# Kernel tuning notes

Hardware: AMD Instinct MI355X
Metric: run time of the kernel (lower is better)

## Reference

```python
import jax, jax.numpy as jnp
import numpy as np

D, HS, HE, E, K = 1024, 2048, 1024, 8, 2   # d_model, shared hidden (d_ff//2), expert hidden (d_ff//4), n_experts, top_k
B, T = 4, 1024
N_SHARED = 1


def setup_inputs() -> dict:
    key = jax.random.key(0)
    ks = jax.random.split(key, 9)
    g = lambda k, shape, s: jax.random.normal(k, shape, jnp.float32) * s
    return {
        "x": g(ks[0], (B, T, D), 1.0),
        "t_emb": g(ks[1], (B, D), 1.0),
        "router_W": g(ks[2], (2 * D, E), 0.01),      # torch Linear(2C->E, bias=False), std=0.01 init
        "router_bias": jnp.zeros((E,), jnp.float32),  # load-balance bias buffer
        "w1": g(ks[3], (D, HS), 0.02),                # shared expert SwiGLU
        "w3": g(ks[4], (D, HS), 0.02),
        "w2": g(ks[5], (HS, D), 0.02),
        "W1e": g(ks[6], (E, D, HE), 0.02),            # routed experts, Linear->GELU->Linear
        "W2e": g(ks[7], (E, HE, D), 0.02),
    }


def reference(x, t_emb, router_W, router_bias, w1, w3, w2, W1e, W2e):
    Bb, Tt, C = x.shape
    xf = x.reshape(-1, C)                                              # [N, C]
    tf = jnp.broadcast_to(t_emb[:, None, :], (Bb, Tt, C)).reshape(-1, C)
    N = xf.shape[0]

    shared = (jax.nn.silu(xf @ w1) * (xf @ w3)) @ w2                   # [N, C]

    # router affinity (sigmoid, fp32)
    s = jax.nn.sigmoid((jnp.concatenate([xf, tf], axis=-1) @ router_W).astype(jnp.float32))
    sel_scores = s + router_bias                                       # [N, E]
    _, topk_idx = jax.lax.top_k(sel_scores, K)                         # [N, K]

    # gates normalized over selected raw affinities
    s_sel = jnp.take_along_axis(s, topk_idx, axis=1)                   # [N, K]
    denom = s_sel.sum(axis=1, keepdims=True)
    gates = jnp.where(denom > 1e-9, s_sel / (denom + 1e-9), 1.0 / K).astype(x.dtype)

    # combine weights [N, E]: scatter gates to selected experts
    combine = jnp.zeros((N, E), x.dtype).at[jnp.arange(N)[:, None], topk_idx].add(gates)

    # dense expert evaluation (reference form of grouped GEMM + scatter-combine)
    h = jax.nn.gelu(jnp.einsum('nc,ech->enh', xf, W1e), approximate=False)  # [E, N, He]
    y = jnp.einsum('enh,ehc->enc', h, W2e)                                   # [E, N, C]
    routed = jnp.einsum('ne,enc->nc', combine, y)                            # [N, C]

    return ((shared + routed) / (N_SHARED + K)).reshape(Bb, Tt, C)
```

## Files before the change

kernel.cpp:

```cpp
#include <hip/hip_runtime.h>
#include <hip/hip_bf16.h>
#include <math.h>

#define D_MODEL 1024
#define HS 2048
#define HE 1024
#define NEXP 8
#define NTOK 4096
#define NSLOT 8192

typedef __attribute__((ext_vector_type(4))) float f32x4;
typedef __attribute__((ext_vector_type(8))) short bf16x8;

__device__ __forceinline__ short f2b(float f) {
  __hip_bfloat16 h = __float2bfloat16(f);
  return *reinterpret_cast<short*>(&h);
}
__device__ __forceinline__ float b2f(short s) {
  return __bfloat162float(*reinterpret_cast<__hip_bfloat16*>(&s));
}

__device__ __forceinline__ void gl_lds16(const short* g, short* l) {
  __builtin_amdgcn_global_load_lds(
      (const __attribute__((address_space(1))) void*)g,
      (__attribute__((address_space(3))) void*)l, 16, 0, 0);
}

__device__ __forceinline__ void tr_tile(const float* __restrict__ in,
                                        short* __restrict__ out, int R, int C,
                                        int bx, int by, int bz, int rmap,
                                        float (*tile)[69], int t) {
  const int c0 = bx * 64;
  const int r0 = by * 64;
  const size_t bo = (size_t)bz * R * C;
  const int lr = t >> 4;
  const int lc4 = (t & 15) * 4;
#pragma unroll
  for (int i = 0; i < 4; i++) {
    const float4 v = *(const float4*)&in[bo + (size_t)(r0 + lr + i * 16) * C + c0 + lc4];
    tile[lc4 + 0][lr + i * 16] = v.x;
    tile[lc4 + 1][lr + i * 16] = v.y;
    tile[lc4 + 2][lr + i * 16] = v.z;
    tile[lc4 + 3][lr + i * 16] = v.w;
  }
  __syncthreads();
#pragma unroll
  for (int i = 0; i < 4; i++) {
    const int oc = (t >> 4) + i * 16;
    const int or4 = (t & 15) * 4;
    short4 o;
    o.x = f2b(tile[oc][or4 + 0]);
    o.y = f2b(tile[oc][or4 + 1]);
    o.z = f2b(tile[oc][or4 + 2]);
    o.w = f2b(tile[oc][or4 + 3]);
    const int c = c0 + oc;
    size_t orow;
    if (rmap == 0) orow = bo + (size_t)c * R;
    else orow = (size_t)((c >> 5) * 64 + (rmap == 2 ? 32 : 0) + (c & 31)) * R;
    *(short4*)&out[orow + r0 + or4] = o;
  }
}

__global__ __launch_bounds__(256) void tr_w13(const float* __restrict__ w1,
                                              const float* __restrict__ w3,
                                              short* __restrict__ w13I) {
  __shared__ float tile[64][69];
  const int z = blockIdx.z;
  tr_tile(z ? w3 : w1, w13I, D_MODEL, HS, blockIdx.x, blockIdx.y, 0, z ? 2 : 1,
          tile, threadIdx.x);
}

__global__ __launch_bounds__(256) void tr_w2(const float* __restrict__ w2,
                                             short* __restrict__ w2T) {
  __shared__ float tile[64][69];
  tr_tile(w2, w2T, HS, D_MODEL, blockIdx.x, blockIdx.y, 0, 0, tile, threadIdx.x);
}

__global__ __launch_bounds__(256) void tr_exp(const float* __restrict__ W1e,
                                              const float* __restrict__ W2e,
                                              short* __restrict__ W1eT,
                                              short* __restrict__ W2eT) {
  __shared__ float tile[64][69];
  const int z = blockIdx.z;
  if (z < 8)
    tr_tile(W1e, W1eT, D_MODEL, HE, blockIdx.x, blockIdx.y, z, 0, tile, threadIdx.x);
  else
    tr_tile(W2e, W2eT, HE, D_MODEL, blockIdx.x, blockIdx.y, z - 8, 0, tile, threadIdx.x);
}

__global__ __launch_bounds__(256) void router_kernel(
    const float* __restrict__ x, const float* __restrict__ temb,
    const float* __restrict__ rw, const float* __restrict__ rbias,
    short* __restrict__ xb, int* __restrict__ topk, float* __restrict__ gates) {
  const int t = (blockIdx.x * 256 + threadIdx.x) >> 6;
  const int lane = threadIdx.x & 63;
  const float* xr = x + (size_t)t * D_MODEL;
  const float* tr = temb + (size_t)(t >> 10) * D_MODEL;
  float acc[NEXP] = {};
#pragma unroll
  for (int i = 0; i < 4; i++) {
    const int j = i * 256 + lane * 4;
    const float4 xv = *(const float4*)&xr[j];
    const float4 tv = *(const float4*)&tr[j];
    short4 o;
    o.x = f2b(xv.x); o.y = f2b(xv.y); o.z = f2b(xv.z); o.w = f2b(xv.w);
    *(short4*)&xb[(size_t)t * D_MODEL + j] = o;
    const float* wx = rw + (size_t)j * NEXP;
    const float* wt = rw + (size_t)(D_MODEL + j) * NEXP;
    const float xa[4] = {xv.x, xv.y, xv.z, xv.w};
    const float ta[4] = {tv.x, tv.y, tv.z, tv.w};
#pragma unroll
    for (int u = 0; u < 4; u++)
#pragma unroll
      for (int e = 0; e < NEXP; e++)
        acc[e] += xa[u] * wx[u * NEXP + e] + ta[u] * wt[u * NEXP + e];
  }
#pragma unroll
  for (int off = 32; off; off >>= 1)
#pragma unroll
    for (int e = 0; e < NEXP; e++) acc[e] += __shfl_xor(acc[e], off);
  if (lane == 0) {
    float s[NEXP], sel[NEXP];
#pragma unroll
    for (int e = 0; e < NEXP; e++) {
      s[e] = 1.f / (1.f + expf(-acc[e]));
      sel[e] = s[e] + rbias[e];
    }
    int i0 = 0;
#pragma unroll
    for (int e = 1; e < NEXP; e++) if (sel[e] > sel[i0]) i0 = e;
    int i1 = (i0 == 0) ? 1 : 0;
#pragma unroll
    for (int e = 0; e < NEXP; e++) if (e != i0 && sel[e] > sel[i1]) i1 = e;
    float s0 = s[i0], s1 = s[i1], den = s0 + s1;
    float g0, g1;
    if (den > 1e-9f) { g0 = s0 / (den + 1e-9f); g1 = s1 / (den + 1e-9f); }
    else { g0 = 0.5f; g1 = 0.5f; }
    topk[t * 2] = i0; topk[t * 2 + 1] = i1;
    gates[t * 2] = g0; gates[t * 2 + 1] = g1;
  }
}

__global__ __launch_bounds__(1024) void group_kernel(const int* __restrict__ topk,
                                                     int* __restrict__ perm,
                                                     int* __restrict__ offs,
                                                     int* __restrict__ te,
                                                     int* __restrict__ tm,
                                                     int* __restrict__ ntile) {
  __shared__ int cnt[NEXP], cur[NEXP];
  const int t = threadIdx.x;
  if (t < NEXP) cnt[t] = 0;
  __syncthreads();
  int mye[8];
#pragma unroll
  for (int i = 0; i < 8; i++) {
    mye[i] = topk[i * 1024 + t];
    atomicAdd(&cnt[mye[i]], 1);
  }
  __syncthreads();
  if (t == 0) {
    int a = 0;
    for (int e = 0; e < NEXP; e++) { offs[e] = a; cur[e] = a; a += cnt[e]; }
    offs[NEXP] = a;
    int nt = 0;
    for (int e = 0; e < NEXP; e++)
      for (int m0 = 0; m0 < cnt[e]; m0 += 256) { te[nt] = e; tm[nt] = m0; nt++; }
    ntile[0] = nt;
  }
  __syncthreads();
#pragma unroll
  for (int i = 0; i < 8; i++) {
    int pos = atomicAdd(&cur[mye[i]], 1);
    perm[pos] = i * 1024 + t;
  }
}

template <int MODE>
__global__ __launch_bounds__(512, 1) void moe_gemm_8ph(
    const short* __restrict__ A, const short* __restrict__ B, short* __restrict__ Cout,
    const int* __restrict__ perm, const int* __restrict__ offs,
    const float* __restrict__ gates, const int* __restrict__ te,
    const int* __restrict__ tm, const int* __restrict__ ntile) {
  extern __shared__ short lds[];
  const int td = threadIdx.x;
  int bx, m0, rbeg = 0, rend = 0;
  const short* Bbase;
  if (MODE == 0) {
    const int id = blockIdx.x, xcd = id & 7, slot = id >> 3;
    bx = (xcd & 3) * 4 + (slot & 3);
    m0 = ((xcd >> 2) * 8 + (slot >> 2)) * 256;
    Bbase = B + (size_t)bx * 256 * 1024;
  } else {
    const int id = blockIdx.x;
    const int work = (id & 7) * 20 + (id >> 3);
    const int ty = work >> 2;
    if (ty >= ntile[0]) return;
    bx = work & 3;
    const int e = te[ty];
    m0 = tm[ty];
    rbeg = offs[e]; rend = offs[e + 1];
    Bbase = B + ((size_t)e * 1024 + bx * 256) * 1024;
  }

  const int srow = td >> 3;
  const int colsw8 = ((td & 7) ^ (srow & 7)) * 8;
  const short* ap[2][2];
  const short* bp[2][2];
#pragma unroll
  for (int h = 0; h < 2; h++)
#pragma unroll
    for (int i = 0; i < 2; i++) {
      const int trow = h * 128 + i * 64 + srow;
      int grow;
      if (MODE == 0) grow = m0 + trow;
      else if (MODE == 1) grow = perm[min(rbeg + m0 + trow, rend - 1)] >> 1;
      else grow = min(rbeg + m0 + trow, rend - 1);
      ap[h][i] = A + (size_t)grow * 1024 + colsw8;
      bp[h][i] = Bbase + (size_t)trow * 1024 + colsw8;
    }

#define SU1(t_, b_)                                                        \
  do {                                                                     \
    gl_lds16(bp[0][0] + (t_) * 64, lds + (b_) * 32768 + 16384 + td * 8);   \
    gl_lds16(bp[0][1] + (t_) * 64, lds + (b_) * 32768 + 16384 + 4096 + td * 8); \
  } while (0)
#define SU2(t_, b_)                                                        \
  do {                                                                     \
    gl_lds16(bp[1][0] + (t_) * 64, lds + (b_) * 32768 + 16384 + 8192 + td * 8); \
    gl_lds16(bp[1][1] + (t_) * 64, lds + (b_) * 32768 + 16384 + 8192 + 4096 + td * 8); \
  } while (0)
#define SU3(t_, b_)                                                        \
  do {                                                                     \
    gl_lds16(ap[0][0] + (t_) * 64, lds + (b_) * 32768 + td * 8);           \
    gl_lds16(ap[1][0] + (t_) * 64, lds + (b_) * 32768 + 8192 + td * 8);    \
  } while (0)
#define SU4(t_, b_)                                                        \
  do {                                                                     \
    gl_lds16(ap[0][1] + (t_) * 64, lds + (b_) * 32768 + 4096 + td * 8);    \
    gl_lds16(ap[1][1] + (t_) * 64, lds + (b_) * 32768 + 8192 + 4096 + td * 8); \
  } while (0)

  const int l = td & 63;
  const int wid = td >> 6;
  const int mh = wid >> 2;
  const int wn4 = wid & 3;
  const int lr = l & 15;
  const int bhsel = wn4 >> 1;
  const int bnr = (wn4 & 1) * 64;
  const int swzk0 = ((0 + (l >> 4) * 16) ^ ((l & 7) << 4)) >> 1;
  const int swzk1 = ((64 + (l >> 4) * 16) ^ ((l & 7) << 4)) >> 1;

#define LDA(mf_, swz_) (*(const bf16x8*)&Ah[(unsigned)(((mf_)*16 + lr) * 64) + (swz_)])
#define LDB(nf_, swz_) (*(const bf16x8*)&Bh[(unsigned)((bnr + (nf_)*16 + lr) * 64) + (swz_)])
#define MMROW(mf_, a_)                                                                 \
  acc[mf_][0] = __builtin_amdgcn_mfma_f32_16x16x32_bf16(a_, b0, acc[mf_][0], 0, 0, 0); \
  acc[mf_][1] = __builtin_amdgcn_mfma_f32_16x16x32_bf16(a_, b1, acc[mf_][1], 0, 0, 0); \
  acc[mf_][2] = __builtin_amdgcn_mfma_f32_16x16x32_bf16(a_, b2, acc[mf_][2], 0, 0, 0); \
  acc[mf_][3] = __builtin_amdgcn_mfma_f32_16x16x32_bf16(a_, b3, acc[mf_][3], 0, 0, 0)

#define PH_TAIL                                   \
  __builtin_amdgcn_s_barrier();                   \
  __builtin_amdgcn_s_setprio(1)
#define PH_END                                    \
  __builtin_amdgcn_s_setprio(0);                  \
  __builtin_amdgcn_s_barrier()

  f32x4 acc[8][4] = {};

  SU1(0, 0); SU2(0, 0); SU3(0, 0); SU4(0, 0);
  asm volatile("s_waitcnt vmcnt(2)" ::: "memory");
  __builtin_amdgcn_s_barrier();

  for (int t = 0; t < 16; ++t) {
    const int p = t & 1, q = p ^ 1;
    const short* Ah = lds + p * 32768 + mh * 8192;
    const short* Bh = lds + p * 32768 + 16384 + bhsel * 8192;
    bf16x8 b0, b1, b2, b3, a0, a1, a2, a3;
    b0 = LDB(0, swzk0); b1 = LDB(1, swzk0); b2 = LDB(2, swzk0); b3 = LDB(3, swzk0);
    a0 = LDA(0, swzk0); a1 = LDA(1, swzk0); a2 = LDA(2, swzk0); a3 = LDA(3, swzk0);
    if (t < 15) {
      SU1(t + 1, q); SU2(t + 1, q);
      asm volatile("s_waitcnt vmcnt(4)" ::: "memory");
    } else {
      asm volatile("s_waitcnt vmcnt(0)" ::: "memory");
    }
    PH_TAIL;
    MMROW(0, a0); MMROW(1, a1); MMROW(2, a2); MMROW(3, a3);
    PH_END;
    a0 = LDA(4, swzk0); a1 = LDA(5, swzk0); a2 = LDA(6, swzk0); a3 = LDA(7, swzk0);
    if (t < 15) { SU3(t + 1, q); SU4(t + 1, q); }
    PH_TAIL;
    MMROW(4, a0); MMROW(5, a1); MMROW(6, a2); MMROW(7, a3);
    PH_END;
    b0 = LDB(0, swzk1); b1 = LDB(1, swzk1); b2 = LDB(2, swzk1); b3 = LDB(3, swzk1);
    a0 = LDA(0, swzk1); a1 = LDA(1, swzk1); a2 = LDA(2, swzk1); a3 = LDA(3, swzk1);
    PH_TAIL;
    MMROW(0, a0); MMROW(1, a1); MMROW(2, a2); MMROW(3, a3);
    PH_END;
    a0 = LDA(4, swzk1); a1 = LDA(5, swzk1); a2 = LDA(6, swzk1); a3 = LDA(7, swzk1);
    if (t < 15) asm volatile("s_waitcnt vmcnt(2)" ::: "memory");
    PH_TAIL;
    MMROW(4, a0); MMROW(5, a1); MMROW(6, a2); MMROW(7, a3);
    PH_END;
  }

  const int rsub = (l >> 4) * 4;
  if (MODE == 0) {
#pragma unroll
    for (int mf = 0; mf < 8; mf++)
#pragma unroll
      for (int j = 0; j < 4; j++) {
        const int row = m0 + mh * 128 + mf * 16 + rsub + j;
        short* Up = Cout + (size_t)row * HS + bx * 128 + wn4 * 32 + lr;
#pragma unroll
        for (int nfp = 0; nfp < 2; nfp++) {
          const float a = acc[mf][nfp][j];
          const float b = acc[mf][nfp + 2][j];
          Up[nfp * 16] = f2b(a / (1.f + expf(-a)) * b);
        }
      }
  } else if (MODE == 1) {
#pragma unroll
    for (int mf = 0; mf < 8; mf++)
#pragma unroll
      for (int j = 0; j < 4; j++) {
        const int gi = rbeg + m0 + mh * 128 + mf * 16 + rsub + j;
        if (gi < rend) {
          short* Cp = Cout + (size_t)gi * HE + bx * 256 + wn4 * 64 + lr;
#pragma unroll
          for (int nf = 0; nf < 4; nf++) {
            const float v = acc[mf][nf][j];
            Cp[nf * 16] = f2b(0.5f * v * (1.0f + erff(v * 0.70710678118654752f)));
          }
        }
      }
  } else {
#pragma unroll
    for (int mf = 0; mf < 8; mf++)
#pragma unroll
      for (int j = 0; j < 4; j++) {
        const int gi = rbeg + m0 + mh * 128 + mf * 16 + rsub + j;
        if (gi < rend) {
          const int slot = perm[gi];
          const float g = gates[slot];
          short* Cp = Cout + (size_t)slot * D_MODEL + bx * 256 + wn4 * 64 + lr;
#pragma unroll
          for (int nf = 0; nf < 4; nf++) Cp[nf * 16] = f2b(g * acc[mf][nf][j]);
        }
      }
  }
#undef SU1
#undef SU2
#undef SU3
#undef SU4
#undef LDA
#undef LDB
#undef MMROW
#undef PH_TAIL
#undef PH_END
}

__global__ __launch_bounds__(256, 2) void gemm_g2(
    const short* __restrict__ A, const short* __restrict__ B,
    const short* __restrict__ yb, float* __restrict__ out) {
  __shared__ __align__(16) short As[4096];
  __shared__ __align__(16) short Bs[4096];
  const int t = threadIdx.x;
  const int id = blockIdx.x, xcd = id & 7, slot = id >> 3;
  const int tile_n = (slot & 7) * 128;
  const int m0 = (xcd * 4 + (slot >> 3)) * 128;
  const int r = t >> 2;
  const int c8 = (t & 3) * 8;
  const short* Ap0 = A + (size_t)(m0 + r) * HS + c8;
  const short* Ap1 = A + (size_t)(m0 + 64 + r) * HS + c8;
  const short* Bp0 = B + (size_t)(tile_n + r) * HS + c8;
  const short* Bp1 = B + (size_t)(tile_n + 64 + r) * HS + c8;

  const int lane = t & 63, wv = t >> 6;
  const int wm = (wv >> 1) * 64, wn = (wv & 1) * 64;
  const int lr = lane & 15, lk = (lane >> 4) * 8;

  f32x4 acc[4][4] = {};
  for (int k0 = 0; k0 < HS; k0 += 32) {
    gl_lds16(Ap0 + k0, &As[t * 8]);
    gl_lds16(Ap1 + k0, &As[2048 + t * 8]);
    gl_lds16(Bp0 + k0, &Bs[t * 8]);
    gl_lds16(Bp1 + k0, &Bs[2048 + t * 8]);
    __syncthreads();
    bf16x8 af[4], bfr[4];
#pragma unroll
    for (int m = 0; m < 4; m++) af[m] = *(const bf16x8*)&As[(wm + m * 16 + lr) * 32 + lk];
#pragma unroll
    for (int n = 0; n < 4; n++) bfr[n] = *(const bf16x8*)&Bs[(wn + n * 16 + lr) * 32 + lk];
#pragma unroll
    for (int m = 0; m < 4; m++)
#pragma unroll
      for (int n = 0; n < 4; n++)
        acc[m][n] = __builtin_amdgcn_mfma_f32_16x16x32_bf16(af[m], bfr[n], acc[m][n], 0, 0, 0);
    __syncthreads();
  }

  const int rq = (lane >> 4) * 4;
  const float inv3 = 1.0f / 3.0f;
#pragma unroll
  for (int m = 0; m < 4; m++) {
#pragma unroll
    for (int j = 0; j < 4; j++) {
      const int tok = m0 + wm + m * 16 + rq + j;
      const int colb = tile_n + wn + lr;
      const short* y0p = yb + (size_t)(tok * 2) * D_MODEL + colb;
      const short* y1p = yb + (size_t)(tok * 2 + 1) * D_MODEL + colb;
      float* Op = out + (size_t)tok * D_MODEL + colb;
#pragma unroll
      for (int n = 0; n < 4; n++) {
        Op[n * 16] = (acc[m][n][j] + b2f(y0p[n * 16]) + b2f(y1p[n * 16])) * inv3;
      }
    }
  }
}

extern "C" void kernel_launch(void* const* d_in, const int* in_sizes, int n_in,
                              void* d_out, int out_size, void* d_ws, size_t ws_size,
                              hipStream_t stream) {
  const float* x = (const float*)d_in[0];
  const float* temb = (const float*)d_in[1];
  const float* rw = (const float*)d_in[2];
  const float* rbias = (const float*)d_in[3];
  const float* w1 = (const float*)d_in[4];
  const float* w3 = (const float*)d_in[5];
  const float* w2 = (const float*)d_in[6];
  const float* W1e = (const float*)d_in[7];
  const float* W2e = (const float*)d_in[8];
  float* out = (float*)d_out;

  const size_t MB = 1ull << 20;
  char* w = (char*)d_ws;
  short* xb    = (short*)(w + 0 * MB);
  short* w13I  = (short*)(w + 8 * MB);
  short* w2T   = (short*)(w + 16 * MB);
  short* W1eT  = (short*)(w + 20 * MB);
  short* W2eT  = (short*)(w + 36 * MB);
  short* ubuf  = (short*)(w + 52 * MB);
  short* hexpb = (short*)(w + 68 * MB);
  short* yb    = (short*)(w + 84 * MB);
  float* gates = (float*)(w + 100 * MB);
  int* topk    = (int*)(w + 100 * MB + 32 * 1024);
  int* perm    = (int*)(w + 100 * MB + 64 * 1024);
  int* meta    = (int*)(w + 100 * MB + 96 * 1024);
  int* offs    = meta;
  int* te      = meta + 16;
  int* tm      = meta + 128;
  int* ntile   = meta + 256;

  hipFuncSetAttribute((const void*)&moe_gemm_8ph<0>,
                      hipFuncAttributeMaxDynamicSharedMemorySize, 131072);
  hipFuncSetAttribute((const void*)&moe_gemm_8ph<1>,
                      hipFuncAttributeMaxDynamicSharedMemorySize, 131072);
  hipFuncSetAttribute((const void*)&moe_gemm_8ph<2>,
                      hipFuncAttributeMaxDynamicSharedMemorySize, 131072);

  tr_w13<<<dim3(HS / 64, D_MODEL / 64, 2), 256, 0, stream>>>(w1, w3, w13I);
  tr_w2<<<dim3(D_MODEL / 64, HS / 64, 1), 256, 0, stream>>>(w2, w2T);
  tr_exp<<<dim3(16, 16, 16), 256, 0, stream>>>(W1e, W2e, W1eT, W2eT);
  router_kernel<<<NTOK / 4, 256, 0, stream>>>(x, temb, rw, rbias, xb, topk, gates);
  group_kernel<<<1, 1024, 0, stream>>>(topk, perm, offs, te, tm, ntile);

  moe_gemm_8ph<0><<<256, 512, 131072, stream>>>(xb, w13I, ubuf, nullptr, nullptr,
                                                nullptr, nullptr, nullptr, nullptr);

  moe_gemm_8ph<1><<<160, 512, 131072, stream>>>(xb, W1eT, hexpb, perm, offs,
                                                gates, te, tm, ntile);
  moe_gemm_8ph<2><<<160, 512, 131072, stream>>>(hexpb, W2eT, yb, perm, offs,
                                                gates, te, tm, ntile);

  gemm_g2<<<256, 256, 0, stream>>>(ubuf, w2T, yb, out);
}
```

Baseline: 236.3 us.

## Restructure GEMM pipelines: coarse per-tile staging and double-buffered swizzled final GEMM

The main MoE GEMM kernel drops its 8-phase interleaved schedule, with barriers after every MFMA group. It now issues all global-to-LDS loads for the next K tile up front, uses one barrier per tile, and runs the MFMA phases without intermediate barriers. The final shared-expert down-projection GEMM is rewritten from a single-buffered 32-wide K loop with two __syncthreads per step into a double-buffered 64-wide K loop with XOR-swizzled LDS and the same coarse staging. This removes barrier overhead and adds load/compute overlap in the final GEMM. In exchange, the finer load/MFMA interleaving in the main kernel is lost, and the final GEMM needs 64KB of dynamic LDS.

```diff
diff --git a/kernel.cpp b/kernel.cpp
--- a/kernel.cpp
+++ b/kernel.cpp
@@ -176,7 +176,7 @@
 }
 
 template <int MODE>
-__global__ __launch_bounds__(512, 1) void moe_gemm_8ph(
+__global__ __launch_bounds__(512, 1) void moe_gemm_ct(
     const short* __restrict__ A, const short* __restrict__ B, short* __restrict__ Cout,
     const int* __restrict__ perm, const int* __restrict__ offs,
     const float* __restrict__ gates, const int* __restrict__ te,
@@ -219,25 +219,16 @@
       bp[h][i] = Bbase + (size_t)trow * 1024 + colsw8;
     }
 
-#define SU1(t_, b_)                                                        \
-  do {                                                                     \
-    gl_lds16(bp[0][0] + (t_) * 64, lds + (b_) * 32768 + 16384 + td * 8);   \
+#define STAGE_ALL(t_, b_)                                                       \
+  do {                                                                          \
+    gl_lds16(bp[0][0] + (t_) * 64, lds + (b_) * 32768 + 16384 + td * 8);        \
     gl_lds16(bp[0][1] + (t_) * 64, lds + (b_) * 32768 + 16384 + 4096 + td * 8); \
-  } while (0)
-#define SU2(t_, b_)                                                        \
-  do {                                                                     \
     gl_lds16(bp[1][0] + (t_) * 64, lds + (b_) * 32768 + 16384 + 8192 + td * 8); \
-    gl_lds16(bp[1][1] + (t_) * 64, lds + (b_) * 32768 + 16384 + 8192 + 4096 + td * 8); \
-  } while (0)
-#define SU3(t_, b_)                                                        \
-  do {                                                                     \
-    gl_lds16(ap[0][0] + (t_) * 64, lds + (b_) * 32768 + td * 8);           \
-    gl_lds16(ap[1][0] + (t_) * 64, lds + (b_) * 32768 + 8192 + td * 8);    \
-  } while (0)
-#define SU4(t_, b_)                                                        \
-  do {                                                                     \
-    gl_lds16(ap[0][1] + (t_) * 64, lds + (b_) * 32768 + 4096 + td * 8);    \
-    gl_lds16(ap[1][1] + (t_) * 64, lds + (b_) * 32768 + 8192 + 4096 + td * 8); \
+    gl_lds16(bp[1][1] + (t_) * 64, lds + (b_) * 32768 + 16384 + 12288 + td * 8);\
+    gl_lds16(ap[0][0] + (t_) * 64, lds + (b_) * 32768 + td * 8);                \
+    gl_lds16(ap[0][1] + (t_) * 64, lds + (b_) * 32768 + 4096 + td * 8);         \
+    gl_lds16(ap[1][0] + (t_) * 64, lds + (b_) * 32768 + 8192 + td * 8);         \
+    gl_lds16(ap[1][1] + (t_) * 64, lds + (b_) * 32768 + 12288 + td * 8);        \
   } while (0)
 
   const int l = td & 63;
@@ -258,50 +249,44 @@
   acc[mf_][2] = __builtin_amdgcn_mfma_f32_16x16x32_bf16(a_, b2, acc[mf_][2], 0, 0, 0); \
   acc[mf_][3] = __builtin_amdgcn_mfma_f32_16x16x32_bf16(a_, b3, acc[mf_][3], 0, 0, 0)
 
-#define PH_TAIL                                   \
-  __builtin_amdgcn_s_barrier();                   \
-  __builtin_amdgcn_s_setprio(1)
-#define PH_END                                    \
-  __builtin_amdgcn_s_setprio(0);                  \
-  __builtin_amdgcn_s_barrier()
-
   f32x4 acc[8][4] = {};
 
-  SU1(0, 0); SU2(0, 0); SU3(0, 0); SU4(0, 0);
-  asm volatile("s_waitcnt vmcnt(2)" ::: "memory");
-  __builtin_amdgcn_s_barrier();
+  STAGE_ALL(0, 0);
 
   for (int t = 0; t < 16; ++t) {
     const int p = t & 1, q = p ^ 1;
     const short* Ah = lds + p * 32768 + mh * 8192;
     const short* Bh = lds + p * 32768 + 16384 + bhsel * 8192;
-    bf16x8 b0, b1, b2, b3, a0, a1, a2, a3;
-    b0 = LDB(0, swzk0); b1 = LDB(1, swzk0); b2 = LDB(2, swzk0); b3 = LDB(3, swzk0);
-    a0 = LDA(0, swzk0); a1 = LDA(1, swzk0); a2 = LDA(2, swzk0); a3 = LDA(3, swzk0);
     if (t < 15) {
-      SU1(t + 1, q); SU2(t + 1, q);
-      asm volatile("s_waitcnt vmcnt(4)" ::: "memory");
+      STAGE_ALL(t + 1, q);
+      asm volatile("s_waitcnt vmcnt(8)" ::: "memory");
     } else {
       asm volatile("s_waitcnt vmcnt(0)" ::: "memory");
     }
-    PH_TAIL;
-    MMROW(0, a0); MMROW(1, a1); MMROW(2, a2); MMROW(3, a3);
-    PH_END;
-    a0 = LDA(4, swzk0); a1 = LDA(5, swzk0); a2 = LDA(6, swzk0); a3 = LDA(7, swzk0);
-    if (t < 15) { SU3(t + 1, q); SU4(t + 1, q); }
-    PH_TAIL;
-    MMROW(4, a0); MMROW(5, a1); MMROW(6, a2); MMROW(7, a3);
-    PH_END;
-    b0 = LDB(0, swzk1); b1 = LDB(1, swzk1); b2 = LDB(2, swzk1); b3 = LDB(3, swzk1);
-    a0 = LDA(0, swzk1); a1 = LDA(1, swzk1); a2 = LDA(2, swzk1); a3 = LDA(3, swzk1);
-    PH_TAIL;
-    MMROW(0, a0); MMROW(1, a1); MMROW(2, a2); MMROW(3, a3);
-    PH_END;
-    a0 = LDA(4, swzk1); a1 = LDA(5, swzk1); a2 = LDA(6, swzk1); a3 = LDA(7, swzk1);
-    if (t < 15) asm volatile("s_waitcnt vmcnt(2)" ::: "memory");
-    PH_TAIL;
-    MMROW(4, a0); MMROW(5, a1); MMROW(6, a2); MMROW(7, a3);
-    PH_END;
+    __builtin_amdgcn_s_barrier();
+    {
+      bf16x8 b0, b1, b2, b3, a0, a1, a2, a3;
+      b0 = LDB(0, swzk0); b1 = LDB(1, swzk0); b2 = LDB(2, swzk0); b3 = LDB(3, swzk0);
+      a0 = LDA(0, swzk0); a1 = LDA(1, swzk0); a2 = LDA(2, swzk0); a3 = LDA(3, swzk0);
+      __builtin_amdgcn_s_setprio(1);
+      MMROW(0, a0); MMROW(1, a1); MMROW(2, a2); MMROW(3, a3);
+      __builtin_amdgcn_s_setprio(0);
+      a0 = LDA(4, swzk0); a1 = LDA(5, swzk0); a2 = LDA(6, swzk0); a3 = LDA(7, swzk0);
+      __builtin_amdgcn_s_setprio(1);
+      MMROW(4, a0); MMROW(5, a1); MMROW(6, a2); MMROW(7, a3);
+      __builtin_amdgcn_s_setprio(0);
+      b0 = LDB(0, swzk1); b1 = LDB(1, swzk1); b2 = LDB(2, swzk1); b3 = LDB(3, swzk1);
+      a0 = LDA(0, swzk1); a1 = LDA(1, swzk1); a2 = LDA(2, swzk1); a3 = LDA(3, swzk1);
+      __builtin_amdgcn_s_setprio(1);
+      MMROW(0, a0); MMROW(1, a1); MMROW(2, a2); MMROW(3, a3);
+      __builtin_amdgcn_s_setprio(0);
+      a0 = LDA(4, swzk1); a1 = LDA(5, swzk1); a2 = LDA(6, swzk1); a3 = LDA(7, swzk1);
+      __builtin_amdgcn_s_setprio(1);
+      MMROW(4, a0); MMROW(5, a1); MMROW(6, a2); MMROW(7, a3);
+      __builtin_amdgcn_s_setprio(0);
+    }
+    __builtin_amdgcn_sched_barrier(0);
+    __builtin_amdgcn_s_barrier();
   }
 
   const int rsub = (l >> 4) * 4;
@@ -349,58 +334,90 @@
         }
       }
   }
-#undef SU1
-#undef SU2
-#undef SU3
-#undef SU4
+#undef STAGE_ALL
 #undef LDA
 #undef LDB
 #undef MMROW
-#undef PH_TAIL
-#undef PH_END
-}
-
-__global__ __launch_bounds__(256, 2) void gemm_g2(
+}
+
+__global__ __launch_bounds__(256, 2) void gemm_g2_ct(
     const short* __restrict__ A, const short* __restrict__ B,
     const short* __restrict__ yb, float* __restrict__ out) {
-  __shared__ __align__(16) short As[4096];
-  __shared__ __align__(16) short Bs[4096];
-  const int t = threadIdx.x;
+  extern __shared__ short lds[];
+  const int td = threadIdx.x;
   const int id = blockIdx.x, xcd = id & 7, slot = id >> 3;
   const int tile_n = (slot & 7) * 128;
   const int m0 = (xcd * 4 + (slot >> 3)) * 128;
-  const int r = t >> 2;
-  const int c8 = (t & 3) * 8;
-  const short* Ap0 = A + (size_t)(m0 + r) * HS + c8;
-  const short* Ap1 = A + (size_t)(m0 + 64 + r) * HS + c8;
-  const short* Bp0 = B + (size_t)(tile_n + r) * HS + c8;
-  const short* Bp1 = B + (size_t)(tile_n + 64 + r) * HS + c8;
-
-  const int lane = t & 63, wv = t >> 6;
+
+  const int srow = td >> 3;
+  const int colsw8 = ((td & 7) ^ (srow & 7)) * 8;
+  const short* ap[4];
+  const short* bp[4];
+#pragma unroll
+  for (int u = 0; u < 4; u++) {
+    ap[u] = A + (size_t)(m0 + u * 32 + srow) * HS + colsw8;
+    bp[u] = B + (size_t)(tile_n + u * 32 + srow) * HS + colsw8;
+  }
+
+#define STAGE_ALL2(t_, b_)                                                 \
+  do {                                                                     \
+    gl_lds16(ap[0] + (t_) * 64, lds + (b_) * 16384 + td * 8);              \
+    gl_lds16(ap[1] + (t_) * 64, lds + (b_) * 16384 + 2048 + td * 8);       \
+    gl_lds16(ap[2] + (t_) * 64, lds + (b_) * 16384 + 4096 + td * 8);       \
+    gl_lds16(ap[3] + (t_) * 64, lds + (b_) * 16384 + 6144 + td * 8);       \
+    gl_lds16(bp[0] + (t_) * 64, lds + (b_) * 16384 + 8192 + td * 8);       \
+    gl_lds16(bp[1] + (t_) * 64, lds + (b_) * 16384 + 10240 + td * 8);      \
+    gl_lds16(bp[2] + (t_) * 64, lds + (b_) * 16384 + 12288 + td * 8);      \
+    gl_lds16(bp[3] + (t_) * 64, lds + (b_) * 16384 + 14336 + td * 8);      \
+  } while (0)
+
+  const int l = td & 63;
+  const int wv = td >> 6;
   const int wm = (wv >> 1) * 64, wn = (wv & 1) * 64;
-  const int lr = lane & 15, lk = (lane >> 4) * 8;
+  const int lr = l & 15;
+  const int swzk0 = ((0 + (l >> 4) * 16) ^ ((l & 7) << 4)) >> 1;
+  const int swzk1 = ((64 + (l >> 4) * 16) ^ ((l & 7) << 4)) >> 1;
+
+#define LDA2(mf_, swz_) (*(const bf16x8*)&Ah[(unsigned)(((mf_)*16 + lr) * 64) + (swz_)])
+#define LDB2(nf_, swz_) (*(const bf16x8*)&Bh[(unsigned)(((nf_)*16 + lr) * 64) + (swz_)])
+#define MMROW2(mf_, a_)                                                                \
+  acc[mf_][0] = __builtin_amdgcn_mfma_f32_16x16x32_bf16(a_, b0, acc[mf_][0], 0, 0, 0); \
+  acc[mf_][1] = __builtin_amdgcn_mfma_f32_16x16x32_bf16(a_, b1, acc[mf_][1], 0, 0, 0); \
+  acc[mf_][2] = __builtin_amdgcn_mfma_f32_16x16x32_bf16(a_, b2, acc[mf_][2], 0, 0, 0); \
+  acc[mf_][3] = __builtin_amdgcn_mfma_f32_16x16x32_bf16(a_, b3, acc[mf_][3], 0, 0, 0)
 
   f32x4 acc[4][4] = {};
-  for (int k0 = 0; k0 < HS; k0 += 32) {
-    gl_lds16(Ap0 + k0, &As[t * 8]);
-    gl_lds16(Ap1 + k0, &As[2048 + t * 8]);
-    gl_lds16(Bp0 + k0, &Bs[t * 8]);
-    gl_lds16(Bp1 + k0, &Bs[2048 + t * 8]);
-    __syncthreads();
-    bf16x8 af[4], bfr[4];
-#pragma unroll
-    for (int m = 0; m < 4; m++) af[m] = *(const bf16x8*)&As[(wm + m * 16 + lr) * 32 + lk];
-#pragma unroll
-    for (int n = 0; n < 4; n++) bfr[n] = *(const bf16x8*)&Bs[(wn + n * 16 + lr) * 32 + lk];
-#pragma unroll
-    for (int m = 0; m < 4; m++)
-#pragma unroll
-      for (int n = 0; n < 4; n++)
-        acc[m][n] = __builtin_amdgcn_mfma_f32_16x16x32_bf16(af[m], bfr[n], acc[m][n], 0, 0, 0);
-    __syncthreads();
-  }
-
-  const int rq = (lane >> 4) * 4;
+
+  STAGE_ALL2(0, 0);
+  for (int t = 0; t < 32; ++t) {
+    const int p = t & 1, q = p ^ 1;
+    const short* Ah = lds + p * 16384 + wm * 64;
+    const short* Bh = lds + p * 16384 + 8192 + wn * 64;
+    if (t < 31) {
+      STAGE_ALL2(t + 1, q);
+      asm volatile("s_waitcnt vmcnt(8)" ::: "memory");
+    } else {
+      asm volatile("s_waitcnt vmcnt(0)" ::: "memory");
+    }
+    __builtin_amdgcn_s_barrier();
+    {
+      bf16x8 b0, b1, b2, b3, a0, a1, a2, a3;
+      b0 = LDB2(0, swzk0); b1 = LDB2(1, swzk0); b2 = LDB2(2, swzk0); b3 = LDB2(3, swzk0);
+      a0 = LDA2(0, swzk0); a1 = LDA2(1, swzk0); a2 = LDA2(2, swzk0); a3 = LDA2(3, swzk0);
+      __builtin_amdgcn_s_setprio(1);
+      MMROW2(0, a0); MMROW2(1, a1); MMROW2(2, a2); MMROW2(3, a3);
+      __builtin_amdgcn_s_setprio(0);
+      b0 = LDB2(0, swzk1); b1 = LDB2(1, swzk1); b2 = LDB2(2, swzk1); b3 = LDB2(3, swzk1);
+      a0 = LDA2(0, swzk1); a1 = LDA2(1, swzk1); a2 = LDA2(2, swzk1); a3 = LDA2(3, swzk1);
+      __builtin_amdgcn_s_setprio(1);
+      MMROW2(0, a0); MMROW2(1, a1); MMROW2(2, a2); MMROW2(3, a3);
+      __builtin_amdgcn_s_setprio(0);
+    }
+    __builtin_amdgcn_sched_barrier(0);
+    __builtin_amdgcn_s_barrier();
+  }
+
+  const int rq = (l >> 4) * 4;
   const float inv3 = 1.0f / 3.0f;
 #pragma unroll
   for (int m = 0; m < 4; m++) {
@@ -417,6 +434,10 @@
       }
     }
   }
+#undef STAGE_ALL2
+#undef LDA2
+#undef LDB2
+#undef MMROW2
 }
 
 extern "C" void kernel_launch(void* const* d_in, const int* in_sizes, int n_in,
@@ -452,12 +473,14 @@
   int* tm      = meta + 128;
   int* ntile   = meta + 256;
 
-  hipFuncSetAttribute((const void*)&moe_gemm_8ph<0>,
+  hipFuncSetAttribute((const void*)&moe_gemm_ct<0>,
                       hipFuncAttributeMaxDynamicSharedMemorySize, 131072);
-  hipFuncSetAttribute((const void*)&moe_gemm_8ph<1>,
+  hipFuncSetAttribute((const void*)&moe_gemm_ct<1>,
                       hipFuncAttributeMaxDynamicSharedMemorySize, 131072);
-  hipFuncSetAttribute((const void*)&moe_gemm_8ph<2>,
+  hipFuncSetAttribute((const void*)&moe_gemm_ct<2>,
                       hipFuncAttributeMaxDynamicSharedMemorySize, 131072);
+  hipFuncSetAttribute((const void*)&gemm_g2_ct,
+                      hipFuncAttributeMaxDynamicSharedMemorySize, 65536);
 
   tr_w13<<<dim3(HS / 64, D_MODEL / 64, 2), 256, 0, stream>>>(w1, w3, w13I);
   tr_w2<<<dim3(D_MODEL / 64, HS / 64, 1), 256, 0, stream>>>(w2, w2T);
@@ -465,13 +488,13 @@
   router_kernel<<<NTOK / 4, 256, 0, stream>>>(x, temb, rw, rbias, xb, topk, gates);
   group_kernel<<<1, 1024, 0, stream>>>(topk, perm, offs, te, tm, ntile);
 
-  moe_gemm_8ph<0><<<256, 512, 131072, stream>>>(xb, w13I, ubuf, nullptr, nullptr,
-                                                nullptr, nullptr, nullptr, nullptr);
-
-  moe_gemm_8ph<1><<<160, 512, 131072, stream>>>(xb, W1eT, hexpb, perm, offs,
-                                                gates, te, tm, ntile);
-  moe_gemm_8ph<2><<<160, 512, 131072, stream>>>(hexpb, W2eT, yb, perm, offs,
-                                                gates, te, tm, ntile);
-
-  gemm_g2<<<256, 256, 0, stream>>>(ubuf, w2T, yb, out);
-}
+  moe_gemm_ct<0><<<256, 512, 131072, stream>>>(xb, w13I, ubuf, nullptr, nullptr,
+                                               nullptr, nullptr, nullptr, nullptr);
+
+  moe_gemm_ct<1><<<160, 512, 131072, stream>>>(xb, W1eT, hexpb, perm, offs,
+                                               gates, te, tm, ntile);
+  moe_gemm_ct<2><<<160, 512, 131072, stream>>>(hexpb, W2eT, yb, perm, offs,
+                                               gates, te, tm, ntile);
+
+  gemm_g2_ct<<<256, 256, 65536, stream>>>(ubuf, w2T, yb, out);
+}
```

Result: faster. 225.7 us (-4.5%).
